# Performance work log

Measured on AMD Instinct MI355X. Metric: run time of the kernel, lower is better.

## Reference

```python
import math
import jax, jax.numpy as jnp
import numpy as np

B, S, D, H = 2, 2048, 1024, 16
DH = D // H
DFF = 4 * D
EPS = 1e-6
MASKED_BIAS = -10000.0


def _gelu(x):
    # GPT-2 tanh-approx GELU
    return 0.5 * x * (1.0 + jnp.tanh(math.sqrt(2.0 / math.pi) * (x + 0.044715 * x ** 3)))


def _layernorm(x, w, b):
    mean = jnp.mean(x, axis=-1, keepdims=True)
    var = jnp.mean((x - mean) ** 2, axis=-1, keepdims=True)
    return w * ((x - mean) / jnp.sqrt(var + EPS)) + b


def setup_inputs() -> dict:
    key = jax.random.key(0)
    ks = jax.random.split(key, 6)
    std = 0.02
    return {
        "hidden_states": jax.random.normal(ks[0], (B, S, D), jnp.float32),
        "w_attn": jax.random.normal(ks[1], (D, 3 * D), jnp.float32) * std,
        "b_attn": jnp.zeros((3 * D,), jnp.float32),
        "w_proj": jax.random.normal(ks[2], (D, D), jnp.float32) * std,
        "b_proj": jnp.zeros((D,), jnp.float32),
        "w_fc": jax.random.normal(ks[3], (D, DFF), jnp.float32) * std,
        "b_fc": jnp.zeros((DFF,), jnp.float32),
        "w_fc_proj": jax.random.normal(ks[4], (DFF, D), jnp.float32) * std,
        "b_fc_proj": jnp.zeros((D,), jnp.float32),
        "ln1_w": jnp.ones((D,), jnp.float32),
        "ln1_b": jnp.zeros((D,), jnp.float32),
        "ln2_w": jnp.ones((D,), jnp.float32),
        "ln2_b": jnp.zeros((D,), jnp.float32),
    }


def reference(hidden_states, w_attn, b_attn, w_proj, b_proj, w_fc, b_fc,
              w_fc_proj, b_fc_proj, ln1_w, ln1_b, ln2_w, ln2_b):
    residual = hidden_states
    x = _layernorm(hidden_states, ln1_w, ln1_b)

    # c_attn: [B,S,D] @ [D,3D] + b -> split into q,k,v
    qkv = x @ w_attn + b_attn
    q, k, v = jnp.split(qkv, 3, axis=-1)
    # split heads -> [B,H,S,DH]
    q = q.reshape(B, S, H, DH).transpose(0, 2, 1, 3)
    k = k.reshape(B, S, H, DH).transpose(0, 2, 1, 3)
    v = v.reshape(B, S, H, DH).transpose(0, 2, 1, 3)

    scores = jnp.einsum('bhqd,bhkd->bhqk', q, k) / jnp.sqrt(jnp.float32(DH))
    causal = jnp.tril(jnp.ones((S, S), bool))  # [S,S]
    scores = jnp.where(causal[None, None], scores, jnp.float32(MASKED_BIAS))
    attn = jax.nn.softmax(scores, axis=-1)
    out = jnp.einsum('bhqk,bhkd->bhqd', attn, v)
    out = out.transpose(0, 2, 1, 3).reshape(B, S, D)
    out = out @ w_proj + b_proj

    h = residual + out
    residual = h
    y = _layernorm(h, ln2_w, ln2_b)
    y = _gelu(y @ w_fc + b_fc)
    y = y @ w_fc_proj + b_fc_proj
    return residual + y
```

## Files before the change

kernel.cpp:

```cpp
#include <hip/hip_runtime.h>
#include <cstdint>
#include <cstddef>

typedef unsigned short u16;
typedef float  floatx4 __attribute__((ext_vector_type(4)));
typedef short  short8  __attribute__((ext_vector_type(8)));
typedef u16    usx4    __attribute__((ext_vector_type(4)));
typedef u16    usx8    __attribute__((ext_vector_type(8)));
typedef unsigned uintx2 __attribute__((ext_vector_type(2)));

__device__ __forceinline__ u16 f2b(float f) {
  unsigned u = __float_as_uint(f);
  unsigned r = u + 0x7fffu + ((u >> 16) & 1u);
  return (u16)(r >> 16);
}
__device__ __forceinline__ float b2f(u16 s) {
  return __uint_as_float(((unsigned)s) << 16);
}

__device__ __forceinline__ unsigned cvt_pk_bf16(float lo, float hi) {
  unsigned r;
  asm("v_cvt_pk_bf16_f32 %0, %1, %2" : "=v"(r) : "v"(lo), "v"(hi));
  return r;
}

__device__ __forceinline__ float rowmax16(float x) {
  int xi = __float_as_int(x), y;
  y = __builtin_amdgcn_update_dpp(xi, xi, 0xB1, 0xF, 0xF, false);
  x = fmaxf(x, __int_as_float(y)); xi = __float_as_int(x);
  y = __builtin_amdgcn_update_dpp(xi, xi, 0x4E, 0xF, 0xF, false);
  x = fmaxf(x, __int_as_float(y)); xi = __float_as_int(x);
  y = __builtin_amdgcn_update_dpp(xi, xi, 0x141, 0xF, 0xF, false);
  x = fmaxf(x, __int_as_float(y)); xi = __float_as_int(x);
  y = __builtin_amdgcn_update_dpp(xi, xi, 0x140, 0xF, 0xF, false);
  x = fmaxf(x, __int_as_float(y));
  return x;
}

__device__ __forceinline__ float gelu_f(float x) {
  const float k = 2.3022082f;
  float u = x * (1.0f + 0.044715f * x * x);
  float t = __builtin_amdgcn_exp2f(-k * u);
  return x * __builtin_amdgcn_rcpf(1.0f + t);
}

__device__ __forceinline__ void gl2lds16(const u16* g, u16* l) {
  __builtin_amdgcn_global_load_lds(
      (const __attribute__((address_space(1))) unsigned int*)g,
      (__attribute__((address_space(3))) unsigned int*)l, 16, 0, 0);
}

#define C2SCALE 0.18033688011112042f

__global__ __launch_bounds__(256) void ln_bf16_kernel(
    const float* __restrict__ in, const float* __restrict__ w,
    const float* __restrict__ b, u16* __restrict__ out)
{
  const int row = blockIdx.x;
  const int t = threadIdx.x;
  const float* p = in + (size_t)row * 1024 + t * 4;
  floatx4 v = *(const floatx4*)p;
  float s  = v.x + v.y + v.z + v.w;
  float ss = v.x*v.x + v.y*v.y + v.z*v.z + v.w*v.w;
  #pragma unroll
  for (int m = 1; m < 64; m <<= 1) {
    s  += __shfl_xor(s,  m);
    ss += __shfl_xor(ss, m);
  }
  __shared__ float red[8];
  if ((t & 63) == 0) { red[(t >> 6)*2] = s; red[(t >> 6)*2 + 1] = ss; }
  __syncthreads();
  s  = red[0] + red[2] + red[4] + red[6];
  ss = red[1] + red[3] + red[5] + red[7];
  const float mean = s * (1.0f / 1024.0f);
  const float var  = ss * (1.0f / 1024.0f) - mean * mean;
  const float rstd = rsqrtf(var + 1e-6f);
  floatx4 wv = *(const floatx4*)(w + t * 4);
  floatx4 bv = *(const floatx4*)(b + t * 4);
  usx4 o = { f2b(wv.x * ((v.x - mean) * rstd) + bv.x),
             f2b(wv.y * ((v.y - mean) * rstd) + bv.y),
             f2b(wv.z * ((v.z - mean) * rstd) + bv.z),
             f2b(wv.w * ((v.w - mean) * rstd) + bv.w) };
  *(usx4*)(out + (size_t)row * 1024 + t * 4) = o;
}

__global__ __launch_bounds__(256) void combine_ln_kernel(
    const u16* __restrict__ p0, const u16* __restrict__ p1,
    const float* __restrict__ res, const float* __restrict__ bias,
    const float* __restrict__ w, const float* __restrict__ b,
    float* __restrict__ hout, u16* __restrict__ yout)
{
  const int row = blockIdx.x;
  const int t = threadIdx.x;
  const size_t i0 = (size_t)row * 1024 + t * 4;
  floatx4 rv = *(const floatx4*)(res + i0);
  usx4 a = *(const usx4*)(p0 + i0);
  usx4 c = *(const usx4*)(p1 + i0);
  floatx4 biasv = *(const floatx4*)(bias + t * 4);
  floatx4 v;
  #pragma unroll
  for (int i = 0; i < 4; ++i) v[i] = rv[i] + b2f(a[i]) + b2f(c[i]) + biasv[i];
  *(floatx4*)(hout + i0) = v;

  float s  = v.x + v.y + v.z + v.w;
  float ss = v.x*v.x + v.y*v.y + v.z*v.z + v.w*v.w;
  #pragma unroll
  for (int m = 1; m < 64; m <<= 1) {
    s  += __shfl_xor(s,  m);
    ss += __shfl_xor(ss, m);
  }
  __shared__ float red[8];
  if ((t & 63) == 0) { red[(t >> 6)*2] = s; red[(t >> 6)*2 + 1] = ss; }
  __syncthreads();
  s  = red[0] + red[2] + red[4] + red[6];
  ss = red[1] + red[3] + red[5] + red[7];
  const float mean = s * (1.0f / 1024.0f);
  const float var  = ss * (1.0f / 1024.0f) - mean * mean;
  const float rstd = rsqrtf(var + 1e-6f);
  floatx4 wv = *(const floatx4*)(w + t * 4);
  floatx4 bv = *(const floatx4*)(b + t * 4);
  usx4 o = { f2b(wv.x * ((v.x - mean) * rstd) + bv.x),
             f2b(wv.y * ((v.y - mean) * rstd) + bv.y),
             f2b(wv.z * ((v.z - mean) * rstd) + bv.z),
             f2b(wv.w * ((v.w - mean) * rstd) + bv.w) };
  *(usx4*)(yout + i0) = o;
}

__device__ __forceinline__ void wtrans_body(
    const float* __restrict__ in, u16* __restrict__ out, int K, int N,
    int bx, int by, int tx, int ty)
{
  __shared__ u16 tile[32][33];
  const int n0 = bx * 32, k0 = by * 32;
  #pragma unroll
  for (int i = 0; i < 4; ++i)
    tile[ty + i*8][tx] = f2b(in[(size_t)(k0 + ty + i*8) * N + n0 + tx]);
  __syncthreads();
  #pragma unroll
  for (int i = 0; i < 4; ++i)
    out[(size_t)(n0 + ty + i*8) * K + k0 + tx] = tile[tx][ty + i*8];
}

__global__ __launch_bounds__(256) void wtrans4_kernel(
    const float* __restrict__ w0, const float* __restrict__ w1,
    const float* __restrict__ w2, const float* __restrict__ w3,
    u16* __restrict__ o0, u16* __restrict__ o1,
    u16* __restrict__ o2, u16* __restrict__ o3)
{
  int blk = blockIdx.x;
  const int tx = threadIdx.x & 31, ty = threadIdx.x >> 5;
  if (blk < 3072) {
    wtrans_body(w0, o0, 1024, 3072, blk % 96, blk / 96, tx, ty);
  } else if (blk < 4096) {
    blk -= 3072; wtrans_body(w1, o1, 1024, 1024, blk % 32, blk / 32, tx, ty);
  } else if (blk < 8192) {
    blk -= 4096; wtrans_body(w2, o2, 1024, 4096, blk % 128, blk / 128, tx, ty);
  } else {
    blk -= 8192; wtrans_body(w3, o3, 4096, 1024, blk % 32, blk / 32, tx, ty);
  }
}

template<int BM, int BN, int FLAGS, int MINW,
         int NX, int NY, int NZ, int RX, int RY, int RZ>
__global__ __launch_bounds__(256, MINW) void gemm_mfma_kernel(
    const u16* __restrict__ A, const u16* __restrict__ Bt,
    const float* __restrict__ bias, const float* __restrict__ Res,
    void* __restrict__ Cout, int M, int N, int K, int kLen, size_t zStride)
{
  constexpr int WM = BM / 2, WN = BN / 2;
  constexpr int MT = WM / 16, NT = WN / 16;
  constexpr int GX = NX / RX, GY = NY / RY, GZ = NZ / RZ;
  __shared__ u16 As[2 * BM * 32];
  __shared__ u16 Bs[2 * BN * 32];

  const int lin = blockIdx.x + NX * (blockIdx.y + NY * blockIdx.z);
  const int xcd = lin & 7;
  const int idx = lin >> 3;
  const int rx = xcd % RX, ry = (xcd / RX) % RY, rz = xcd / (RX * RY);
  const int bx = rx * GX + idx % GX;
  const int by = ry * GY + (idx / GX) % GY;
  const int bz = rz * GZ + idx / (GX * GY);

  const int t = threadIdx.x;
  const int wave = t >> 6, lane = t & 63;
  const int quad = lane >> 4, l16 = lane & 15;
  const int wm = wave >> 1, wn = wave & 1;
  const int bm0 = by * BM, bn0 = bx * BN;
  const int kStart = bz * kLen;

  const int sRow = lane >> 2;
  const int sq   = (lane & 3) ^ ((lane >> 4) & 3);

  const u16* aG[BM / 64];
  u16* aL[BM / 64];
  #pragma unroll
  for (int j = 0; j < BM / 64; ++j) {
    const int band = j * 4 + wave;
    aG[j] = A + (size_t)(bm0 + band * 16 + sRow) * K + kStart + sq * 8;
    aL[j] = As + band * 512;
  }
  const u16* bG[BN / 64];
  u16* bL[BN / 64];
  #pragma unroll
  for (int j = 0; j < BN / 64; ++j) {
    const int band = j * 4 + wave;
    bG[j] = Bt + (size_t)(bn0 + band * 16 + sRow) * K + kStart + sq * 8;
    bL[j] = Bs + band * 512;
  }

  floatx4 acc[MT][NT] = {};
  const int rcol = (quad ^ (l16 >> 2)) << 3;

  auto stage = [&](int koff, int buf) {
    #pragma unroll
    for (int j = 0; j < BM / 64; ++j) gl2lds16(aG[j] + koff, aL[j] + buf * (BM * 32));
    #pragma unroll
    for (int j = 0; j < BN / 64; ++j) gl2lds16(bG[j] + koff, bL[j] + buf * (BN * 32));
  };
  auto compute = [&](const u16* Asc, const u16* Bsc) {
    short8 af[MT], bf[NT];
    #pragma unroll
    for (int mt = 0; mt < MT; ++mt)
      af[mt] = *(const short8*)&Asc[(wm*WM + mt*16 + l16) * 32 + rcol];
    #pragma unroll
    for (int nt = 0; nt < NT; ++nt)
      bf[nt] = *(const short8*)&Bsc[(wn*WN + nt*16 + l16) * 32 + rcol];
    #pragma unroll
    for (int mt = 0; mt < MT; ++mt)
      #pragma unroll
      for (int nt = 0; nt < NT; ++nt)
        acc[mt][nt] = __builtin_amdgcn_mfma_f32_16x16x32_bf16(af[mt], bf[nt], acc[mt][nt], 0, 0, 0);
  };

  stage(0, 0);
  for (int k0 = 0; k0 < kLen; k0 += 64) {
    __syncthreads();
    stage(k0 + 32, 1);
    compute(As, Bs);
    __syncthreads();
    if (k0 + 64 < kLen) stage(k0 + 64, 0);
    compute(As + BM * 32, Bs + BN * 32);
  }

  const int orow0 = bm0 + wm * WM;
  const int ocol0 = bn0 + wn * WN;
  const size_t zoff = (size_t)bz * zStride;
  #pragma unroll
  for (int nt = 0; nt < NT; ++nt) {
    const int col = ocol0 + nt*16 + l16;
    const float bv = bias ? bias[col] : 0.0f;
    const float postscale = ((FLAGS & 8) && col < 1024) ? C2SCALE : 1.0f;
    #pragma unroll
    for (int mt = 0; mt < MT; ++mt) {
      #pragma unroll
      for (int r = 0; r < 4; ++r) {
        const int row = orow0 + mt*16 + quad*4 + r;
        float v = acc[mt][nt][r] + bv;
        if (FLAGS & 1) v = gelu_f(v);
        if (FLAGS & 8) v *= postscale;
        if (FLAGS & 2) v += Res[(size_t)row * N + col];
        if (FLAGS & 4) ((u16*)Cout)[zoff + (size_t)row * N + col] = f2b(v);
        else           ((float*)Cout)[zoff + (size_t)row * N + col] = v;
      }
    }
  }
}

__global__ __launch_bounds__(256, 4) void attn_mfma_kernel(
    const u16* __restrict__ qkv, u16* __restrict__ opart, float* __restrict__ ml)
{
  __shared__ u16 Ks[64][72];
  __shared__ u16 Vt[64][72];
  __shared__ u16 Ps[64][72];

  const int t    = threadIdx.x;
  const int wave = t >> 6;
  const int lane = t & 63;
  const int quad = lane >> 4;
  const int l16  = lane & 15;
  const int pair = blockIdx.x >> 1;
  const int half = blockIdx.x & 1;
  const int h    = blockIdx.y;
  const int b    = blockIdx.z;

  const size_t base = (size_t)b * 2048 * 3072;
  const int qoff = h * 64;
  const int koff = 1024 + h * 64;
  const int voff = 2048 + h * 64;

  const int prow = t >> 2;
  const int scol = (t & 3) * 16;
  const int kmap = ((prow & 15) << 2) | (prow >> 4);
  const int kpair  = t & 31;
  const int vchunk = t >> 5;

  const size_t obase  = ((((size_t)half * 2 + b) * 16 + h) * 2048) * 64;
  const size_t mlbase = ((((size_t)half * 2 + b) * 16 + h) * 2048) * 2;

  short8 onesb;
  {
    const short v = (l16 == 0) ? (short)0x3F80 : (short)0;
    #pragma unroll
    for (int i = 0; i < 8; ++i) onesb[i] = v;
  }

  #pragma unroll 1
  for (int iter = 0; iter < 2; ++iter) {
    const int qi = iter ? (31 - pair) : pair;
    const int q0 = qi << 6;
    const int T  = qi + 1;
    const int mid = (T + 1) >> 1;
    const int t0 = half ? mid : 0;
    const int t1 = half ? T : mid;

    floatx4 of[4] = {};
    floatx4 ofl = {};
    float m[4];
    #pragma unroll
    for (int r = 0; r < 4; ++r) m[r] = -1e30f;

    if (t0 < t1) {
      __syncthreads();
      {
        const u16* qp = qkv + base + (size_t)(q0 + prow) * 3072 + qoff + scol;
        *(usx8*)&Ks[prow][scol]     = *(const usx8*)qp;
        *(usx8*)&Ks[prow][scol + 8] = *(const usx8*)(qp + 8);
      }
      __syncthreads();
      const short8 qf0 = *(const short8*)&Ks[wave*16 + l16][quad*8];
      const short8 qf1 = *(const short8*)&Ks[wave*16 + l16][32 + quad*8];

      usx8 kr0, kr1, vr0, vr1;
      {
        const int k0 = t0 << 6;
        const u16* kp = qkv + base + (size_t)(k0 + kmap) * 3072 + koff + scol;
        kr0 = *(const usx8*)kp; kr1 = *(const usx8*)(kp + 8);
        const u16* vp = qkv + base + (size_t)(k0 + 2*kpair) * 3072 + voff + vchunk*8;
        vr0 = *(const usx8*)vp; vr1 = *(const usx8*)(vp + 3072);
      }

      for (int tIdx = t0; tIdx < t1; ++tIdx) {
        __syncthreads();
        *(usx8*)&Ks[prow][scol]     = kr0;
        *(usx8*)&Ks[prow][scol + 8] = kr1;
        #pragma unroll
        for (int i = 0; i < 8; ++i)
          *(unsigned*)&Vt[vchunk*8 + i][2*kpair] =
              (unsigned)vr0[i] | ((unsigned)vr1[i] << 16);
        __syncthreads();

        if (tIdx + 1 < t1) {
          const int kn = (tIdx + 1) << 6;
          const u16* kp = qkv + base + (size_t)(kn + kmap) * 3072 + koff + scol;
          kr0 = *(const usx8*)kp; kr1 = *(const usx8*)(kp + 8);
          const u16* vp = qkv + base + (size_t)(kn + 2*kpair) * 3072 + voff + vchunk*8;
          vr0 = *(const usx8*)vp; vr1 = *(const usx8*)(vp + 3072);
        }

        const int k0 = tIdx << 6;
        floatx4 sf[4];
        #pragma unroll
        for (int kt = 0; kt < 4; ++kt) {
          short8 kf0 = *(const short8*)&Ks[kt*16 + l16][quad*8];
          short8 kf1 = *(const short8*)&Ks[kt*16 + l16][32 + quad*8];
          floatx4 z = {};
          z      = __builtin_amdgcn_mfma_f32_16x16x32_bf16(qf0, kf0, z, 0, 0, 0);
          sf[kt] = __builtin_amdgcn_mfma_f32_16x16x32_bf16(qf1, kf1, z, 0, 0, 0);
        }

        const bool diag = (tIdx == qi);
        #pragma unroll
        for (int r = 0; r < 4; ++r) {
          float sv0 = sf[0][r], sv1 = sf[1][r], sv2 = sf[2][r], sv3 = sf[3][r];
          if (diag) {
            const int qrow = q0 + wave*16 + quad*4 + r;
            const int kbase = k0 + 4*l16;
            if (kbase     > qrow) sv0 = -1e30f;
            if (kbase + 1 > qrow) sv1 = -1e30f;
            if (kbase + 2 > qrow) sv2 = -1e30f;
            if (kbase + 3 > qrow) sv3 = -1e30f;
          }
          float mx = fmaxf(fmaxf(sv0, sv1), fmaxf(sv2, sv3));
          mx = rowmax16(mx);
          const float nm = fmaxf(m[r], mx);
          const float alpha = __builtin_amdgcn_exp2f(m[r] - nm);
          m[r] = nm;
          const float p0 = __builtin_amdgcn_exp2f(sv0 - nm);
          const float p1 = __builtin_amdgcn_exp2f(sv1 - nm);
          const float p2 = __builtin_amdgcn_exp2f(sv2 - nm);
          const float p3 = __builtin_amdgcn_exp2f(sv3 - nm);
          uintx2 pw = { cvt_pk_bf16(p0, p1), cvt_pk_bf16(p2, p3) };
          *(uintx2*)&Ps[wave*16 + quad*4 + r][l16 * 4] = pw;
          #pragma unroll
          for (int dht = 0; dht < 4; ++dht) of[dht][r] *= alpha;
          ofl[r] *= alpha;
        }

        short8 pf0 = *(const short8*)&Ps[wave*16 + l16][quad*8];
        short8 pf1 = *(const short8*)&Ps[wave*16 + l16][32 + quad*8];
        #pragma unroll
        for (int dht = 0; dht < 4; ++dht) {
          short8 vf0 = *(const short8*)&Vt[dht*16 + l16][quad*8];
          short8 vf1 = *(const short8*)&Vt[dht*16 + l16][32 + quad*8];
          of[dht] = __builtin_amdgcn_mfma_f32_16x16x32_bf16(pf0, vf0, of[dht], 0, 0, 0);
          of[dht] = __builtin_amdgcn_mfma_f32_16x16x32_bf16(pf1, vf1, of[dht], 0, 0, 0);
        }
        ofl = __builtin_amdgcn_mfma_f32_16x16x32_bf16(pf0, onesb, ofl, 0, 0, 0);
        ofl = __builtin_amdgcn_mfma_f32_16x16x32_bf16(pf1, onesb, ofl, 0, 0, 0);
      }
    }

    #pragma unroll
    for (int r = 0; r < 4; ++r) {
      const int s = q0 + wave*16 + quad*4 + r;
      u16* orow = opart + obase + (size_t)s * 64;
      #pragma unroll
      for (int dht = 0; dht < 4; ++dht) orow[dht*16 + l16] = f2b(of[dht][r]);
      const float lr = __shfl(ofl[r], quad * 16);
      if (l16 == 0) { ml[mlbase + 2*s] = m[r]; ml[mlbase + 2*s + 1] = lr; }
    }
  }
}

__global__ __launch_bounds__(256) void attn_combine_kernel(
    const u16* __restrict__ opart, const float* __restrict__ ml,
    u16* __restrict__ out)
{
  const int t = threadIdx.x;
  const int s = blockIdx.x * 4 + (t >> 6);
  const int lane = t & 63;
  const int h = blockIdx.y, b = blockIdx.z;

  const size_t o0  = ((((size_t)0 * 2 + b) * 16 + h) * 2048 + s) * 64 + lane;
  const size_t o1  = ((((size_t)1 * 2 + b) * 16 + h) * 2048 + s) * 64 + lane;
  const size_t ml0 = ((((size_t)0 * 2 + b) * 16 + h) * 2048 + s) * 2;
  const size_t ml1 = ((((size_t)1 * 2 + b) * 16 + h) * 2048 + s) * 2;

  const float m0 = ml[ml0], l0 = ml[ml0 + 1];
  const float m1 = ml[ml1], l1 = ml[ml1 + 1];
  const float M  = fmaxf(m0, m1);
  const float w0 = __builtin_amdgcn_exp2f(m0 - M);
  const float w1 = __builtin_amdgcn_exp2f(m1 - M);
  const float L  = w0 * l0 + w1 * l1;
  const float o  = w0 * b2f(opart[o0]) + w1 * b2f(opart[o1]);
  out[((size_t)b * 2048 + s) * 1024 + h * 64 + lane] = f2b(o / L);
}

__global__ __launch_bounds__(256) void ksplit_combine_kernel(
    const u16* __restrict__ p0, const u16* __restrict__ p1,
    const float* __restrict__ res, const float* __restrict__ bias,
    float* __restrict__ out)
{
  const size_t i0 = ((size_t)blockIdx.x * 256 + threadIdx.x) * 8;
  usx8 a = *(const usx8*)(p0 + i0);
  usx8 c = *(const usx8*)(p1 + i0);
  const int col = (int)(i0 & 1023);
  floatx4 bv0 = *(const floatx4*)(bias + col);
  floatx4 bv1 = *(const floatx4*)(bias + col + 4);
  floatx4 h0 = *(const floatx4*)(res + i0);
  floatx4 h1 = *(const floatx4*)(res + i0 + 4);
  floatx4 o0, o1;
  #pragma unroll
  for (int i = 0; i < 4; ++i) o0[i] = h0[i] + b2f(a[i])   + b2f(c[i])   + bv0[i];
  #pragma unroll
  for (int i = 0; i < 4; ++i) o1[i] = h1[i] + b2f(a[4+i]) + b2f(c[4+i]) + bv1[i];
  *(floatx4*)(out + i0)     = o0;
  *(floatx4*)(out + i0 + 4) = o1;
}

extern "C" void kernel_launch(void* const* d_in, const int* in_sizes, int n_in,
                              void* d_out, int out_size, void* d_ws, size_t ws_size,
                              hipStream_t stream) {
  const float* hidden    = (const float*)d_in[0];
  const float* w_attn    = (const float*)d_in[1];
  const float* b_attn    = (const float*)d_in[2];
  const float* w_proj    = (const float*)d_in[3];
  const float* b_proj    = (const float*)d_in[4];
  const float* w_fc      = (const float*)d_in[5];
  const float* b_fc      = (const float*)d_in[6];
  const float* w_fc_proj = (const float*)d_in[7];
  const float* b_fc_proj = (const float*)d_in[8];
  const float* ln1_w     = (const float*)d_in[9];
  const float* ln1_b     = (const float*)d_in[10];
  const float* ln2_w     = (const float*)d_in[11];
  const float* ln2_b     = (const float*)d_in[12];

  char* wsb = (char*)d_ws;
  u16*   qkvb  = (u16*)  (wsb + (size_t)( 0u << 20));
  u16*   xb    = (u16*)  (wsb + (size_t)(24u << 20));
  u16*   opart = (u16*)  (wsb + (size_t)(24u << 20));
  float* mlbuf = (float*)(wsb + (size_t)(40u << 20));
  u16*   attnb = (u16*)  (wsb + (size_t)(42u << 20));
  u16*   wqT   = (u16*)  (wsb + (size_t)(50u << 20));
  u16*   wpT   = (u16*)  (wsb + (size_t)(56u << 20));
  u16*   wfT   = (u16*)  (wsb + (size_t)(58u << 20));
  u16*   wfpT  = (u16*)  (wsb + (size_t)(66u << 20));
  u16*   pproj = (u16*)  (wsb + (size_t)(24u << 20));
  float* hbuf  = (float*)(wsb + (size_t)(42u << 20));
  u16*   yb    = (u16*)  (wsb + (size_t)( 0u << 20));
  u16*   fcb   = (u16*)  (wsb + (size_t)( 8u << 20));
  u16*   pfcp0 = (u16*)  (wsb + (size_t)( 0u << 20));
  u16*   pfcp1 = (u16*)  (wsb + (size_t)(58u << 20));
  const size_t zstr_fcp = ((size_t)58u << 20) / 2;

  wtrans4_kernel<<<dim3(12288), 256, 0, stream>>>(
      w_attn, w_proj, w_fc, w_fc_proj, wqT, wpT, wfT, wfpT);

  ln_bf16_kernel<<<4096, 256, 0, stream>>>(hidden, ln1_w, ln1_b, xb);
  gemm_mfma_kernel<128,128,12,4, 24,32,1, 2,4,1><<<dim3(24, 32, 1), 256, 0, stream>>>(
      xb, wqT, b_attn, nullptr, qkvb, 4096, 3072, 1024, 1024, 0);
  attn_mfma_kernel<<<dim3(32, 16, 2), 256, 0, stream>>>(qkvb, opart, mlbuf);
  attn_combine_kernel<<<dim3(512, 16, 2), 256, 0, stream>>>(opart, mlbuf, attnb);
  gemm_mfma_kernel<128,64,4,4, 16,32,2, 1,4,2><<<dim3(16, 32, 2), 256, 0, stream>>>(
      attnb, wpT, nullptr, nullptr, pproj, 4096, 1024, 1024, 512, 4194304);
  combine_ln_kernel<<<4096, 256, 0, stream>>>(
      pproj, pproj + 4194304, hidden, b_proj, ln2_w, ln2_b, hbuf, yb);
  gemm_mfma_kernel<128,128,5,4, 32,32,1, 2,4,1><<<dim3(32, 32, 1), 256, 0, stream>>>(
      yb, wfT, b_fc, nullptr, fcb, 4096, 4096, 1024, 1024, 0);
  gemm_mfma_kernel<128,64,4,4, 16,32,2, 1,4,2><<<dim3(16, 32, 2), 256, 0, stream>>>(
      fcb, wfpT, nullptr, nullptr, pfcp0, 4096, 1024, 4096, 2048, zstr_fcp);
  ksplit_combine_kernel<<<dim3(2048), 256, 0, stream>>>(
      pfcp0, pfcp1, hbuf, b_fc_proj, (float*)d_out);
}
```

Measured before the change: 352.3 us.

## Triple-buffer GEMM LDS staging with vmcnt-based waits and MFMA priority

Replaces the double-buffered GEMM main loop with a three-stage LDS ring. Each step issues the load for two tiles ahead and waits with a partial s_waitcnt vmcnt plus a barrier, rather than two full __syncthreads per 64-wide K step. MFMA sections are raised with s_setprio so they are favoured over other waves. The aim is to hide global-to-LDS latency and halve the barrier count. It costs 50% more LDS, and the 128x128 GEMMs lower their min-waves launch bound from 4 to 3, which may reduce occupancy.

```diff
diff --git a/kernel.cpp b/kernel.cpp
--- a/kernel.cpp
+++ b/kernel.cpp
@@ -48,6 +48,12 @@
   __builtin_amdgcn_global_load_lds(
       (const __attribute__((address_space(1))) unsigned int*)g,
       (__attribute__((address_space(3))) unsigned int*)l, 16, 0, 0);
+}
+
+template<int N> __device__ __forceinline__ void wait_stage_barrier() {
+  asm volatile("s_waitcnt vmcnt(%0)" :: "n"(N) : "memory");
+  __builtin_amdgcn_s_barrier();
+  __builtin_amdgcn_sched_barrier(0);
 }
 
 #define C2SCALE 0.18033688011112042f
@@ -170,8 +176,10 @@
   constexpr int WM = BM / 2, WN = BN / 2;
   constexpr int MT = WM / 16, NT = WN / 16;
   constexpr int GX = NX / RX, GY = NY / RY, GZ = NZ / RZ;
-  __shared__ u16 As[2 * BM * 32];
-  __shared__ u16 Bs[2 * BN * 32];
+  constexpr int ABUF = BM * 32, BBUF = BN * 32;
+  constexpr int L = BM / 64 + BN / 64;
+  __shared__ u16 As[3 * ABUF];
+  __shared__ u16 Bs[3 * BBUF];
 
   const int lin = blockIdx.x + NX * (blockIdx.y + NY * blockIdx.z);
   const int xcd = lin & 7;
@@ -211,13 +219,15 @@
   floatx4 acc[MT][NT] = {};
   const int rcol = (quad ^ (l16 >> 2)) << 3;
 
-  auto stage = [&](int koff, int buf) {
-    #pragma unroll
-    for (int j = 0; j < BM / 64; ++j) gl2lds16(aG[j] + koff, aL[j] + buf * (BM * 32));
-    #pragma unroll
-    for (int j = 0; j < BN / 64; ++j) gl2lds16(bG[j] + koff, bL[j] + buf * (BN * 32));
+  auto stage = [&](int tile, int buf) {
+    #pragma unroll
+    for (int j = 0; j < BM / 64; ++j) gl2lds16(aG[j] + tile * 32, aL[j] + buf * ABUF);
+    #pragma unroll
+    for (int j = 0; j < BN / 64; ++j) gl2lds16(bG[j] + tile * 32, bL[j] + buf * BBUF);
   };
-  auto compute = [&](const u16* Asc, const u16* Bsc) {
+  auto compute = [&](int buf) {
+    const u16* Asc = As + buf * ABUF;
+    const u16* Bsc = Bs + buf * BBUF;
     short8 af[MT], bf[NT];
     #pragma unroll
     for (int mt = 0; mt < MT; ++mt)
@@ -225,29 +235,37 @@
     #pragma unroll
     for (int nt = 0; nt < NT; ++nt)
       bf[nt] = *(const short8*)&Bsc[(wn*WN + nt*16 + l16) * 32 + rcol];
+    __builtin_amdgcn_s_setprio(1);
     #pragma unroll
     for (int mt = 0; mt < MT; ++mt)
       #pragma unroll
       for (int nt = 0; nt < NT; ++nt)
         acc[mt][nt] = __builtin_amdgcn_mfma_f32_16x16x32_bf16(af[mt], bf[nt], acc[mt][nt], 0, 0, 0);
+    __builtin_amdgcn_s_setprio(0);
   };
 
+  const int nt = kLen >> 5;
   stage(0, 0);
-  for (int k0 = 0; k0 < kLen; k0 += 64) {
-    __syncthreads();
-    stage(k0 + 32, 1);
-    compute(As, Bs);
-    __syncthreads();
-    if (k0 + 64 < kLen) stage(k0 + 64, 0);
-    compute(As + BM * 32, Bs + BN * 32);
-  }
+  stage(1, 1);
+  int cur = 0;
+  for (int ti = 0; ti < nt - 1; ++ti) {
+    wait_stage_barrier<L>();
+    if (ti + 2 < nt) {
+      const int sb = cur >= 1 ? cur - 1 : 2;
+      stage(ti + 2, sb);
+    }
+    compute(cur);
+    cur = cur < 2 ? cur + 1 : 0;
+  }
+  wait_stage_barrier<0>();
+  compute(cur);
 
   const int orow0 = bm0 + wm * WM;
   const int ocol0 = bn0 + wn * WN;
   const size_t zoff = (size_t)bz * zStride;
   #pragma unroll
-  for (int nt = 0; nt < NT; ++nt) {
-    const int col = ocol0 + nt*16 + l16;
+  for (int nt2 = 0; nt2 < NT; ++nt2) {
+    const int col = ocol0 + nt2*16 + l16;
     const float bv = bias ? bias[col] : 0.0f;
     const float postscale = ((FLAGS & 8) && col < 1024) ? C2SCALE : 1.0f;
     #pragma unroll
@@ -255,7 +273,7 @@
       #pragma unroll
       for (int r = 0; r < 4; ++r) {
         const int row = orow0 + mt*16 + quad*4 + r;
-        float v = acc[mt][nt][r] + bv;
+        float v = acc[mt][nt2][r] + bv;
         if (FLAGS & 1) v = gelu_f(v);
         if (FLAGS & 8) v *= postscale;
         if (FLAGS & 2) v += Res[(size_t)row * N + col];
@@ -507,7 +525,7 @@
       w_attn, w_proj, w_fc, w_fc_proj, wqT, wpT, wfT, wfpT);
 
   ln_bf16_kernel<<<4096, 256, 0, stream>>>(hidden, ln1_w, ln1_b, xb);
-  gemm_mfma_kernel<128,128,12,4, 24,32,1, 2,4,1><<<dim3(24, 32, 1), 256, 0, stream>>>(
+  gemm_mfma_kernel<128,128,12,3, 24,32,1, 2,4,1><<<dim3(24, 32, 1), 256, 0, stream>>>(
       xb, wqT, b_attn, nullptr, qkvb, 4096, 3072, 1024, 1024, 0);
   attn_mfma_kernel<<<dim3(32, 16, 2), 256, 0, stream>>>(qkvb, opart, mlbuf);
   attn_combine_kernel<<<dim3(512, 16, 2), 256, 0, stream>>>(opart, mlbuf, attnb);
@@ -515,7 +533,7 @@
       attnb, wpT, nullptr, nullptr, pproj, 4096, 1024, 1024, 512, 4194304);
   combine_ln_kernel<<<4096, 256, 0, stream>>>(
       pproj, pproj + 4194304, hidden, b_proj, ln2_w, ln2_b, hbuf, yb);
-  gemm_mfma_kernel<128,128,5,4, 32,32,1, 2,4,1><<<dim3(32, 32, 1), 256, 0, stream>>>(
+  gemm_mfma_kernel<128,128,5,3, 32,32,1, 2,4,1><<<dim3(32, 32, 1), 256, 0, stream>>>(
       yb, wfT, b_fc, nullptr, fcb, 4096, 4096, 1024, 1024, 0);
   gemm_mfma_kernel<128,64,4,4, 16,32,2, 1,4,2><<<dim3(16, 32, 2), 256, 0, stream>>>(
       fcb, wfpT, nullptr, nullptr, pfcp0, 4096, 1024, 4096, 2048, zstr_fcp);
```

Result: slower. 361.0 us (+2.5%).
